# Kernel optimization log

Hardware: AMD Instinct MI355X
Metric: run time of the kernel (lower is better)

## Reference

```python
import jax, jax.numpy as jnp
import numpy as np
import math

# ---- config (matches init_kwargs) ----
C_IN, C_OUT = 256, 256
KH = KW = 3
PAD, STRIDE = 1, 1
CURV = 1.0          # Poincare ball curvature c
SC = math.sqrt(CURV)
EPS = 1e-15
B, H, W = 32, 32, 32
D = C_IN * KH * KW  # 2304, unfolded feature dim


def _beta(a, b):
    # scipy.special.beta via lgamma
    return math.exp(math.lgamma(a) + math.lgamma(b) - math.lgamma(a + b))


def _unfold(x):
    # torch.nn.Unfold: [B,C,H,W] -> [B, C*KH*KW, L], channel-major patch order
    b, c, h, w = x.shape
    xp = jnp.pad(x, ((0, 0), (0, 0), (PAD, PAD), (PAD, PAD)))
    ho = (h + 2 * PAD - KH) // STRIDE + 1
    wo = (w + 2 * PAD - KW) // STRIDE + 1
    patches = [xp[:, :, i:i + STRIDE * ho:STRIDE, j:j + STRIDE * wo:STRIDE]
               for i in range(KH) for j in range(KW)]      # KH*KW slices, each [B,C,ho,wo]
    p = jnp.stack(patches, axis=2)                          # [B, C, KH*KW, ho, wo]
    return p.reshape(b, c * KH * KW, ho * wo), ho, wo


def _expmap0(v):
    # exponential map at origin along last axis: tanh(sc*||v||) v/(sc*||v||)
    n = jnp.sqrt(jnp.maximum(jnp.sum(v * v, axis=-1, keepdims=True), EPS * EPS))
    return jnp.tanh(SC * n) * v / (SC * n)


def _logmap0_chan(y):
    # log map at origin along channel axis (dim=1 of [B,O,H,W])
    n = jnp.sqrt(jnp.maximum(jnp.sum(y * y, axis=1, keepdims=True), EPS * EPS))
    arg = jnp.clip(SC * n, 0.0, 1.0 - 1e-7)
    return jnp.arctanh(arg) * y / (SC * n)


def _poincare_fc(x, z, r):
    # HNN++ Poincare fully-connected. x: [B,L,D] on ball, z: [D,O], r: [O]
    x2 = jnp.sum(x * x, axis=-1, keepdims=True)          # [B,L,1]
    lam = 2.0 / (1.0 - CURV * x2)                        # conformal factor
    zn = jnp.maximum(jnp.linalg.norm(z, axis=0), EPS)    # [O]
    xz = jnp.einsum('bld,do->blo', x, z / zn)            # [B,L,O]
    tcr = 2.0 * SC * r                                   # [O]
    v = (2.0 * zn / SC) * jnp.arcsinh(
        SC * lam * xz * jnp.cosh(tcr) - (lam - 1.0) * jnp.sinh(tcr))
    w = jnp.sinh(SC * v) / SC                            # [B,L,O]
    return w / (1.0 + jnp.sqrt(1.0 + CURV * jnp.sum(w * w, axis=-1, keepdims=True)))


def setup_inputs() -> dict:
    key = jax.random.key(0)
    k1, k2, k3 = jax.random.split(key, 3)
    x = jax.random.normal(k1, (B, C_IN, H, W), jnp.float32) * 0.02
    std = (2.0 * D * C_OUT) ** (-0.5)
    weights = jax.random.normal(k2, (D, C_OUT), jnp.float32) * std
    bias = jax.random.normal(k3, (C_OUT,), jnp.float32) * 0.01
    return {"x": x, "weights": weights, "bias": bias}


def reference(x, weights, bias):
    beta_ni = _beta(C_IN / 2.0, 0.5)
    beta_n = _beta(C_IN * KH * KW / 2.0, 0.5)
    x = x * (beta_n / beta_ni)
    cols, ho, wo = _unfold(x)                # [B, D, L]
    cols = jnp.swapaxes(cols, 1, 2)          # [B, L, D]
    h = _expmap0(cols)                       # map im2col rows onto the ball
    y = _poincare_fc(h, weights, bias)       # [B, L, O]
    y = jnp.swapaxes(y, 1, 2).reshape(x.shape[0], C_OUT, ho, wo)
    return _logmap0_chan(y)                  # [B, O, ho, wo]
```

## Files before the change

### kernel.cpp

```cpp
#include <hip/hip_runtime.h>
#include <cmath>

typedef float f32x4 __attribute__((ext_vector_type(4)));
typedef __bf16 bfx8 __attribute__((ext_vector_type(8)));
typedef const __attribute__((address_space(1))) void g_void;
typedef __attribute__((address_space(3))) void lds_void;

#define B_SZ 32
#define CIN 256
#define HW 32
#define OUTC 256
#define KTOT 2304
#define HP 34
#define M_TOT 32768

#define XP_OFF   0u
#define XP_BYTES 18939904u
#define WT_OFF   (XP_OFF + XP_BYTES)
#define WT_BYTES 1179648u
#define ZN_OFF   (WT_OFF + WT_BYTES)
#define MF_OFF   (ZN_OFF + 1024u)
#define T_OFF    (MF_OFF + 262144u)

#define LDS_A_OFF 0
#define LDS_B_OFF 65536
#define LDS_TAB   98304
#define LDS_TOTAL 104448

__device__ __forceinline__ unsigned short f2bf(float f) {
  union { float f; unsigned u; } v; v.f = f;
  unsigned r = v.u + 0x7FFFu + ((v.u >> 16) & 1u);
  return (unsigned short)(r >> 16);
}

__device__ __forceinline__ void gload16(const void* g, void* l) {
  __builtin_amdgcn_global_load_lds((g_void*)g, (lds_void*)l, 16, 0, 0);
}

__device__ __forceinline__ float asinh_f(float x) { return logf(x + sqrtf(x * x + 1.f)); }
__device__ __forceinline__ float sinh_f(float v)  { float e = expf(v); return 0.5f * (e - 1.f / e); }
__device__ __forceinline__ float atanh_f(float t) { return 0.5f * logf((1.f + t) / (1.f - t)); }

#define MEMBAR() asm volatile("" ::: "memory")
#define RAWBAR() do { MEMBAR(); __builtin_amdgcn_s_barrier(); MEMBAR(); } while (0)

__global__ void k_prep_x(const float* __restrict__ x, unsigned short* __restrict__ xp,
                         float* __restrict__ T, float ratio) {
  __shared__ float tile[256][33];
  __shared__ float red[8][32];
  const int h = blockIdx.x, b = blockIdx.y, t = threadIdx.x;
  const int w = t & 31, g = t >> 5;
  const float* xb = x + ((b * 256) * 32 + h) * 32;
#pragma unroll
  for (int i = 0; i < 32; ++i) {
    int c = i * 8 + g;
    tile[c][w] = xb[c * 1024 + w] * ratio;
  }
  __syncthreads();
  unsigned short* xpb = xp + ((b * HP + h + 1) * HP + 1) * 256 + t;
#pragma unroll 8
  for (int w2 = 0; w2 < 32; ++w2) xpb[w2 * 256] = f2bf(tile[t][w2]);
  float s = 0.f;
#pragma unroll
  for (int j = 0; j < 32; ++j) { float v = tile[g * 32 + j][w]; s += v * v; }
  red[g][w] = s;
  __syncthreads();
  if (t < 32) {
    float a = 0.f;
#pragma unroll
    for (int q = 0; q < 8; ++q) a += red[q][t];
    T[(b * 32 + h) * 32 + t] = a;
  }
}

__global__ void k_rowfac(const float* __restrict__ T, float2* __restrict__ mf) {
  int m = blockIdx.x * 256 + threadIdx.x;
  int b = m >> 10, ohw = m & 1023, oh = ohw >> 5, ow = ohw & 31;
  const float* Tb = T + b * 1024;
  float nv2 = 0.f;
  for (int di = -1; di <= 1; ++di) {
    int hh = oh + di; if (hh < 0 || hh > 31) continue;
    for (int dj = -1; dj <= 1; ++dj) {
      int ww = ow + dj; if (ww < 0 || ww > 31) continue;
      nv2 += Tb[hh * 32 + ww];
    }
  }
  float n = sqrtf(fmaxf(nv2, 1e-30f));
  float th = tanhf(n);
  float hf = th / n;
  float lam = 2.f / fmaxf(1.f - th * th, 1e-12f);
  mf[m] = make_float2(lam * hf, lam - 1.f);
}

__global__ void k_zn(const float* __restrict__ wts, float* __restrict__ zn2) {
  __shared__ float red[256];
  int o = blockIdx.x, t = threadIdx.x;
  float a = 0.f;
#pragma unroll
  for (int j = 0; j < 9; ++j) { float v = wts[(t + j * 256) * 256 + o]; a += v * v; }
  red[t] = a; __syncthreads();
  for (int s = 128; s > 0; s >>= 1) { if (t < s) red[t] += red[t + s]; __syncthreads(); }
  if (t == 0) zn2[o] = red[0];
}

__global__ void k_wt(const float* __restrict__ wts, const float* __restrict__ zn2,
                     unsigned short* __restrict__ Wt) {
  int d = blockIdx.x, o = threadIdx.x;
  float zn = sqrtf(fmaxf(zn2[o], 1e-30f));
  float v = wts[d * 256 + o] / zn;
  int c = d / 9, kk = d - c * 9;
  Wt[o * KTOT + kk * 256 + c] = f2bf(v);
}

__global__ __launch_bounds__(512, 2) void k_gemm(
    const unsigned short* __restrict__ xp, const unsigned short* __restrict__ Wt,
    const float* __restrict__ zn2, const float* __restrict__ bias,
    const float2* __restrict__ mf, float* __restrict__ out) {
  extern __shared__ char smem[];

  const int tid = threadIdx.x;
  const int wid = tid >> 6, lane = tid & 63;
  const int m0 = blockIdx.x * 128;
  const int b = m0 >> 10, ohw0 = m0 & 1023;

  float2* mf_s = (float2*)(smem + LDS_TAB);
  float* zn_s = (float*)(smem + LDS_TAB + 1024);
  float* C_s  = (float*)(smem + LDS_TAB + 2048);
  float* S_s  = (float*)(smem + LDS_TAB + 3072);
  float (*part_s)[128] = (float (*)[128])(smem + LDS_TAB + 4096);

  if (tid < 128) {
    mf_s[tid] = mf[m0 + tid];
  } else if (tid < 384) {
    int o = tid - 128;
    float zn = sqrtf(fmaxf(zn2[o], 1e-30f));
    float e = expf(2.f * bias[o]);
    float ie = 1.f / e;
    zn_s[o] = zn;
    C_s[o] = 0.5f * (e + ie);
    S_s[o] = 0.5f * (e - ie);
  }
  MEMBAR();
  asm volatile("s_waitcnt vmcnt(0) lgkmcnt(0)" ::: "memory");
  __builtin_amdgcn_sched_barrier(0);

  const int kcl = (tid & 7) ^ ((tid >> 3) & 7);
  const unsigned short* wa[4];
#pragma unroll
  for (int j2 = 0; j2 < 4; ++j2) {
    int o = j2 * 64 + (tid >> 3);
    wa[j2] = Wt + o * KTOT + kcl * 8;
  }
  const unsigned short* ib[2];
#pragma unroll
  for (int j = 0; j < 2; ++j) {
    int ml = j * 64 + (tid >> 3);
    int oh = (ohw0 + ml) >> 5, ow = (ohw0 + ml) & 31;
    ib[j] = xp + ((b * HP + oh) * HP + ow) * 256 + kcl * 8;
  }

  const int kq = lane >> 4, l15 = lane & 15;
  const int og = wid >> 1, mg = wid & 1;
  const int xa = l15 & 7;
  const int c0 = ((kq) ^ xa) * 16;
  const int c1 = ((4 + kq) ^ xa) * 16;
  const int ra = (og * 64 + l15) * 128;
  const int rb = (mg * 64 + l15) * 128;

  f32x4 acc[4][4];
#pragma unroll
  for (int i = 0; i < 4; ++i)
#pragma unroll
    for (int j = 0; j < 4; ++j) acc[i][j] = f32x4{0.f, 0.f, 0.f, 0.f};

  auto stage = [&](int t, int buf) {
    const int koff = t * 64;
    char* abase = smem + LDS_A_OFF + buf * 32768 + wid * 1024;
#pragma unroll
    for (int j2 = 0; j2 < 4; ++j2)
      gload16(wa[j2] + koff, abase + j2 * 8192);
    const int p = t >> 2;
    const int di = (p >= 6) ? 2 : ((p >= 3) ? 1 : 0);
    const int dj = p - di * 3;
    const int ioff = (di * HP + dj) * 256 + (t & 3) * 64;
    char* bbase = smem + LDS_B_OFF + buf * 16384 + wid * 1024;
    gload16(ib[0] + ioff, bbase);
    gload16(ib[1] + ioff, bbase + 8192);
  };

  stage(0, 0);
  stage(1, 1);

  for (int t = 0; t < 36; ++t) {
    const int buf = t & 1;
    if (t < 35) asm volatile("s_waitcnt vmcnt(6)" ::: "memory");
    else        asm volatile("s_waitcnt vmcnt(0)" ::: "memory");
    RAWBAR();
    __builtin_amdgcn_sched_barrier(0);

    const char* Abuf = smem + LDS_A_OFF + buf * 32768;
    const char* Bbuf = smem + LDS_B_OFF + buf * 16384;
    bfx8 fa0[4], fa1[4], fb0[4], fb1[4];
#pragma unroll
    for (int oi = 0; oi < 4; ++oi) {
      fa0[oi] = *(const bfx8*)(Abuf + ra + oi * 2048 + c0);
      fa1[oi] = *(const bfx8*)(Abuf + ra + oi * 2048 + c1);
    }
#pragma unroll
    for (int mi = 0; mi < 4; ++mi) {
      fb0[mi] = *(const bfx8*)(Bbuf + rb + mi * 2048 + c0);
      fb1[mi] = *(const bfx8*)(Bbuf + rb + mi * 2048 + c1);
    }

    __builtin_amdgcn_s_setprio(1);
#pragma unroll
    for (int oi = 0; oi < 4; ++oi)
#pragma unroll
      for (int mi = 0; mi < 4; ++mi)
        acc[oi][mi] = __builtin_amdgcn_mfma_f32_16x16x32_bf16(fa0[oi], fb0[mi], acc[oi][mi], 0, 0, 0);
    __builtin_amdgcn_s_setprio(0);

    asm volatile("s_waitcnt lgkmcnt(0)" ::: "memory");
    __builtin_amdgcn_sched_barrier(0);
    RAWBAR();

    if (t < 34) stage(t + 2, buf);

    __builtin_amdgcn_s_setprio(1);
#pragma unroll
    for (int oi = 0; oi < 4; ++oi)
#pragma unroll
      for (int mi = 0; mi < 4; ++mi)
        acc[oi][mi] = __builtin_amdgcn_mfma_f32_16x16x32_bf16(fa1[oi], fb1[mi], acc[oi][mi], 0, 0, 0);
    __builtin_amdgcn_s_setprio(0);
  }

  const int o_base = og * 64, m_base = mg * 64;
#pragma unroll
  for (int oi = 0; oi < 4; ++oi) {
#pragma unroll
    for (int r = 0; r < 4; ++r) {
      int o = o_base + oi * 16 + kq * 4 + r;
      float zn2o = 2.f * zn_s[o], Co = C_s[o], So = S_s[o];
#pragma unroll
      for (int mi = 0; mi < 4; ++mi) {
        int mloc = m_base + mi * 16 + l15;
        float2 f = mf_s[mloc];
        float arg = f.x * acc[oi][mi][r] * Co - f.y * So;
        acc[oi][mi][r] = sinh_f(zn2o * asinh_f(arg));
      }
    }
  }

  float swp[4];
#pragma unroll
  for (int mi = 0; mi < 4; ++mi) {
    float s = 0.f;
#pragma unroll
    for (int oi = 0; oi < 4; ++oi)
#pragma unroll
      for (int r = 0; r < 4; ++r) s += acc[oi][mi][r] * acc[oi][mi][r];
    s += __shfl_xor(s, 16);
    s += __shfl_xor(s, 32);
    swp[mi] = s;
  }
  __syncthreads();
  if (lane < 16) {
#pragma unroll
    for (int mi = 0; mi < 4; ++mi) part_s[og][m_base + mi * 16 + lane] = swp[mi];
  }
  __syncthreads();

  float gm[4];
#pragma unroll
  for (int mi = 0; mi < 4; ++mi) {
    int mloc = m_base + mi * 16 + l15;
    float Sw = part_s[0][mloc] + part_s[1][mloc] + part_s[2][mloc] + part_s[3][mloc];
    float sq = sqrtf(fmaxf(Sw, 1e-30f));
    float s = 1.f / (1.f + sqrtf(1.f + Sw));
    float tt = fminf(s * sq, 1.f - 1e-7f);
    gm[mi] = atanh_f(tt) / sq;
  }

  float* outb = out + (b * 256) * 1024 + ohw0;
#pragma unroll
  for (int oi = 0; oi < 4; ++oi) {
#pragma unroll
    for (int r = 0; r < 4; ++r) {
      int o = o_base + oi * 16 + kq * 4 + r;
      float* op = outb + o * 1024;
#pragma unroll
      for (int mi = 0; mi < 4; ++mi)
        op[m_base + mi * 16 + l15] = acc[oi][mi][r] * gm[mi];
    }
  }
}

extern "C" void kernel_launch(void* const* d_in, const int* in_sizes, int n_in,
                              void* d_out, int out_size, void* d_ws, size_t ws_size,
                              hipStream_t stream) {
  const float* x    = (const float*)d_in[0];
  const float* wts  = (const float*)d_in[1];
  const float* bias = (const float*)d_in[2];
  float* out = (float*)d_out;
  char* ws = (char*)d_ws;
  unsigned short* xp = (unsigned short*)(ws + XP_OFF);
  unsigned short* Wt = (unsigned short*)(ws + WT_OFF);
  float* zn2 = (float*)(ws + ZN_OFF);
  float2* mfv = (float2*)(ws + MF_OFF);
  float* T = (float*)(ws + T_OFF);

  double bni = exp(::lgamma(128.0) + ::lgamma(0.5) - ::lgamma(128.5));
  double bn  = exp(::lgamma(1152.0) + ::lgamma(0.5) - ::lgamma(1152.5));
  float ratio = (float)(bn / bni);

  hipMemsetAsync(xp, 0, XP_BYTES, stream);
  k_prep_x<<<dim3(32, 32), 256, 0, stream>>>(x, xp, T, ratio);
  k_rowfac<<<128, 256, 0, stream>>>(T, mfv);
  k_zn<<<256, 256, 0, stream>>>(wts, zn2);
  k_wt<<<KTOT, 256, 0, stream>>>(wts, zn2, Wt);
  k_gemm<<<256, 512, LDS_TOTAL, stream>>>(xp, Wt, zn2, bias, mfv, out);
}
```

Baseline: 94.20 us.

## Load B operand fragments directly from global into registers, bypassing LDS

The im2col activation tile is no longer staged through LDS. Each lane now loads its MFMA B fragments straight from global memory into registers, double-buffered one K-step ahead, with the vmcnt waits recomputed to match. Only the weight tile still goes through LDS. This removes the LDS writes, reads and shared buffer for B and shrinks LDS use, which may allow more occupancy. In exchange it costs more global load instructions per lane with less coalescing (each lane fetches 16-byte pieces on its own) and more registers for the prefetched fragments.

```diff
diff --git a/kernel.cpp b/kernel.cpp
--- a/kernel.cpp
+++ b/kernel.cpp
@@ -22,10 +22,8 @@
 #define MF_OFF   (ZN_OFF + 1024u)
 #define T_OFF    (MF_OFF + 262144u)
 
-#define LDS_A_OFF 0
-#define LDS_B_OFF 65536
-#define LDS_TAB   98304
-#define LDS_TOTAL 104448
+#define LDS_TAB   65536
+#define LDS_TOTAL 71680
 
 __device__ __forceinline__ unsigned short f2bf(float f) {
   union { float f; unsigned u; } v; v.f = f;
@@ -151,13 +149,6 @@
     int o = j2 * 64 + (tid >> 3);
     wa[j2] = Wt + o * KTOT + kcl * 8;
   }
-  const unsigned short* ib[2];
-#pragma unroll
-  for (int j = 0; j < 2; ++j) {
-    int ml = j * 64 + (tid >> 3);
-    int oh = (ohw0 + ml) >> 5, ow = (ohw0 + ml) & 31;
-    ib[j] = xp + ((b * HP + oh) * HP + ow) * 256 + kcl * 8;
-  }
 
   const int kq = lane >> 4, l15 = lane & 15;
   const int og = wid >> 1, mg = wid & 1;
@@ -165,7 +156,15 @@
   const int c0 = ((kq) ^ xa) * 16;
   const int c1 = ((4 + kq) ^ xa) * 16;
   const int ra = (og * 64 + l15) * 128;
-  const int rb = (mg * 64 + l15) * 128;
+
+  const char* rb[4];
+#pragma unroll
+  for (int mi = 0; mi < 4; ++mi) {
+    int mloc = mg * 64 + mi * 16 + l15;
+    int m = ohw0 + mloc;
+    int oh = m >> 5, ow = m & 31;
+    rb[mi] = (const char*)(xp + ((b * HP + oh) * HP + ow) * 256) + kq * 16;
+  }
 
   f32x4 acc[4][4];
 #pragma unroll
@@ -175,64 +174,69 @@
 
   auto stage = [&](int t, int buf) {
     const int koff = t * 64;
-    char* abase = smem + LDS_A_OFF + buf * 32768 + wid * 1024;
+    char* abase = smem + buf * 32768 + wid * 1024;
 #pragma unroll
     for (int j2 = 0; j2 < 4; ++j2)
       gload16(wa[j2] + koff, abase + j2 * 8192);
+  };
+
+  auto loadfb = [&](bfx8* dst, int t) {
     const int p = t >> 2;
     const int di = (p >= 6) ? 2 : ((p >= 3) ? 1 : 0);
     const int dj = p - di * 3;
-    const int ioff = (di * HP + dj) * 256 + (t & 3) * 64;
-    char* bbase = smem + LDS_B_OFF + buf * 16384 + wid * 1024;
-    gload16(ib[0] + ioff, bbase);
-    gload16(ib[1] + ioff, bbase + 8192);
+    const int off = (di * HP + dj) * 512 + (t & 3) * 128;
+#pragma unroll
+    for (int mi = 0; mi < 4; ++mi) {
+      dst[mi]     = *(const bfx8*)(rb[mi] + off);
+      dst[4 + mi] = *(const bfx8*)(rb[mi] + off + 64);
+    }
   };
 
-  stage(0, 0);
-  stage(1, 1);
-
-  for (int t = 0; t < 36; ++t) {
-    const int buf = t & 1;
-    if (t < 35) asm volatile("s_waitcnt vmcnt(6)" ::: "memory");
-    else        asm volatile("s_waitcnt vmcnt(0)" ::: "memory");
+  auto tile_body = [&](int t, int buf, bfx8* fbc, bfx8* fbn) {
+    if (t < 35) loadfb(fbn, t + 1);
+    MEMBAR(); __builtin_amdgcn_sched_barrier(0);
+    if (t < 35) asm volatile("s_waitcnt vmcnt(20)" ::: "memory");
+    else        asm volatile("s_waitcnt vmcnt(8)"  ::: "memory");
     RAWBAR();
     __builtin_amdgcn_sched_barrier(0);
 
-    const char* Abuf = smem + LDS_A_OFF + buf * 32768;
-    const char* Bbuf = smem + LDS_B_OFF + buf * 16384;
-    bfx8 fa0[4], fa1[4], fb0[4], fb1[4];
+    const char* Abuf = smem + buf * 32768;
+    bfx8 fa0[4], fa1[4];
 #pragma unroll
     for (int oi = 0; oi < 4; ++oi) {
       fa0[oi] = *(const bfx8*)(Abuf + ra + oi * 2048 + c0);
       fa1[oi] = *(const bfx8*)(Abuf + ra + oi * 2048 + c1);
     }
-#pragma unroll
-    for (int mi = 0; mi < 4; ++mi) {
-      fb0[mi] = *(const bfx8*)(Bbuf + rb + mi * 2048 + c0);
-      fb1[mi] = *(const bfx8*)(Bbuf + rb + mi * 2048 + c1);
-    }
-
     __builtin_amdgcn_s_setprio(1);
 #pragma unroll
     for (int oi = 0; oi < 4; ++oi)
 #pragma unroll
       for (int mi = 0; mi < 4; ++mi)
-        acc[oi][mi] = __builtin_amdgcn_mfma_f32_16x16x32_bf16(fa0[oi], fb0[mi], acc[oi][mi], 0, 0, 0);
+        acc[oi][mi] = __builtin_amdgcn_mfma_f32_16x16x32_bf16(fa0[oi], fbc[mi], acc[oi][mi], 0, 0, 0);
     __builtin_amdgcn_s_setprio(0);
-
     asm volatile("s_waitcnt lgkmcnt(0)" ::: "memory");
     __builtin_amdgcn_sched_barrier(0);
     RAWBAR();
-
     if (t < 34) stage(t + 2, buf);
-
+    MEMBAR(); __builtin_amdgcn_sched_barrier(0);
     __builtin_amdgcn_s_setprio(1);
 #pragma unroll
     for (int oi = 0; oi < 4; ++oi)
 #pragma unroll
       for (int mi = 0; mi < 4; ++mi)
-        acc[oi][mi] = __builtin_amdgcn_mfma_f32_16x16x32_bf16(fa1[oi], fb1[mi], acc[oi][mi], 0, 0, 0);
+        acc[oi][mi] = __builtin_amdgcn_mfma_f32_16x16x32_bf16(fa1[oi], fbc[4 + mi], acc[oi][mi], 0, 0, 0);
     __builtin_amdgcn_s_setprio(0);
+  };
+
+  bfx8 fbA[8], fbB[8];
+  stage(0, 0);
+  stage(1, 1);
+  loadfb(fbA, 0);
+  MEMBAR(); __builtin_amdgcn_sched_barrier(0);
+
+  for (int u = 0; u < 18; ++u) {
+    tile_body(2 * u,     0, fbA, fbB);
+    tile_body(2 * u + 1, 1, fbB, fbA);
   }
 
   const int o_base = og * 64, m_base = mg * 64;
```

After: 140.2 us. 1.49x slower.
